# Kernel optimization log

Measured on AMD Instinct MI355X. Metric: run time of the kernel, lower is better.

The kernel has to match this reference:

```python
import jax, jax.numpy as jnp
import numpy as np

N, D, H, N_HEADS = 2048, 512, 512, 16

def setup_inputs() -> dict:
    key = jax.random.key(0)
    k1, k2, k3 = jax.random.split(key, 3)
    inputs = jax.random.normal(k1, (N, D), dtype=jnp.float32)
    idx = jax.random.randint(k2, (N,), 0, N_HEADS, dtype=jnp.int64)
    weights = jax.random.normal(k3, (N_HEADS, D, H), dtype=jnp.float32)
    biases = jnp.zeros((N_HEADS, H), dtype=jnp.float32)
    return {"inputs": inputs, "idx": idx, "weights": weights, "biases": biases}

def reference(inputs, idx, weights, biases):
    # per-sample weight gather: (N, D, H) then batched vec-mat: (N, 1, D) @ (N, D, H) -> (N, H)
    w = weights[idx]            # (N, D, H)  -- the redundant materialized gather
    b = biases[idx]             # (N, H)
    return jnp.einsum('nd,ndh->nh', inputs, w) + b
```

## Files before the change

kernel.cpp:

```cpp
#include <hip/hip_runtime.h>


#define N_SAMPLES 2048
#define DIM       512
#define HDIM      512
#define N_HEADS   16
#define SH        32
#define BPITCH    520

typedef __attribute__((ext_vector_type(8))) short bf16x8;
typedef __attribute__((ext_vector_type(4))) float floatx4;

__device__ inline unsigned short f2bf_rne(float f) {
    union { float f; unsigned u; } v; v.f = f;
    return (unsigned short)((v.u + 0x7FFFu + ((v.u >> 16) & 1u)) >> 16);
}
__device__ inline unsigned bfpack_rne(float lo, float hi) {
    return (unsigned)f2bf_rne(lo) | ((unsigned)f2bf_rne(hi) << 16);
}

__global__ __launch_bounds__(256) void xconv(const float* __restrict__ x,
                                             unsigned* __restrict__ xb) {
    const int i = blockIdx.x * 256 + threadIdx.x;
    const float4 v0 = *(const float4*)(x + i * 8);
    const float4 v1 = *(const float4*)(x + i * 8 + 4);
    uint4 o;
    o.x = bfpack_rne(v0.x, v0.y);
    o.y = bfpack_rne(v0.z, v0.w);
    o.z = bfpack_rne(v1.x, v1.y);
    o.w = bfpack_rne(v1.z, v1.w);
    *(uint4*)(xb + i * 4) = o;
}

__global__ __launch_bounds__(256, 2) void fused(
    const unsigned short* __restrict__ xb,
    const int*   __restrict__ idx,
    const float* __restrict__ w,
    const float* __restrict__ bias,
    float*       __restrict__ out)
{
    __shared__ unsigned short Bl[SH * BPITCH];
    __shared__ unsigned short slist[N_SAMPLES];
    __shared__ int wcnt[4];

    const int bid  = blockIdx.x;
    const int head = bid >> 4;
    const int h0   = (bid & 15) * SH;
    const int t    = threadIdx.x;
    const int wave = t >> 6;
    const int lane = t & 63;
    const int l16  = lane & 15;
    const int quad = lane >> 4;

    int myidx[8];
    #pragma unroll
    for (int c = 0; c < 8; ++c)
        myidx[c] = idx[(wave * 8 + c) * 64 + lane];

    const int hh = (t & 7) * 4;
    const int dg = t >> 3;
    const float* wg = w + (size_t)head * DIM * HDIM + h0;
    float4 q[16];
    #pragma unroll
    for (int s = 0; s < 16; ++s)
        q[s] = *(const float4*)(wg + (size_t)(dg * 16 + s) * HDIM + hh);

    unsigned long long masks[8];
    {
        int mycnt = 0;
        #pragma unroll
        for (int c = 0; c < 8; ++c) {
            masks[c] = __ballot(myidx[c] == head);
            mycnt += __popcll(masks[c]);
        }
        if (lane == 0) wcnt[wave] = mycnt;
    }
    __syncthreads();
    int cnt = 0, base = 0;
    #pragma unroll
    for (int i = 0; i < 4; ++i) { if (i < wave) base += wcnt[i]; cnt += wcnt[i]; }
    {
        int pos = base;
        #pragma unroll
        for (int c = 0; c < 8; ++c) {
            const unsigned long long m = masks[c];
            if (m & (1ull << lane)) {
                const int rank = __popcll(m & ((1ull << lane) - 1ull));
                slist[pos + rank] = (unsigned short)((wave * 8 + c) * 64 + lane);
            }
            pos += __popcll(m);
        }
    }

    #pragma unroll
    for (int p = 0; p < 8; ++p) {
        const int d = dg * 16 + 2 * p;
        const float4 qa = q[2 * p], qb = q[2 * p + 1];
        *(unsigned*)&Bl[(hh + 0) * BPITCH + d] = bfpack_rne(qa.x, qb.x);
        *(unsigned*)&Bl[(hh + 1) * BPITCH + d] = bfpack_rne(qa.y, qb.y);
        *(unsigned*)&Bl[(hh + 2) * BPITCH + d] = bfpack_rne(qa.z, qb.z);
        *(unsigned*)&Bl[(hh + 3) * BPITCH + d] = bfpack_rne(qa.w, qb.w);
    }
    __syncthreads();

    const int   mt  = (cnt + 15) >> 4;
    const float bv0 = bias[head * HDIM + h0 + l16];
    const float bv1 = bias[head * HDIM + h0 + 16 + l16];

    int j = wave;
    bf16x8 a[16];
    if (j < mt) {
        const int mg  = j * 16 + l16;
        const int row = slist[mg < cnt ? mg : cnt - 1];
        const unsigned short* ap = xb + (size_t)row * DIM + quad * 8;
        #pragma unroll
        for (int ks = 0; ks < 16; ++ks) a[ks] = *(const bf16x8*)(ap + ks * 32);
    }
    for (; j < mt; j += 4) {
        bf16x8 an[16];
        const int jn = j + 4;
        if (jn < mt) {
            const int mg  = jn * 16 + l16;
            const int row = slist[mg < cnt ? mg : cnt - 1];
            const unsigned short* ap = xb + (size_t)row * DIM + quad * 8;
            #pragma unroll
            for (int ks = 0; ks < 16; ++ks) an[ks] = *(const bf16x8*)(ap + ks * 32);
        }

        floatx4 acc0 = {0.f, 0.f, 0.f, 0.f};
        floatx4 acc1 = {0.f, 0.f, 0.f, 0.f};
        #pragma unroll
        for (int ks = 0; ks < 16; ++ks) {
            const bf16x8 b0 = *(const bf16x8*)&Bl[l16 * BPITCH + ks * 32 + quad * 8];
            const bf16x8 b1 = *(const bf16x8*)&Bl[(16 + l16) * BPITCH + ks * 32 + quad * 8];
            acc0 = __builtin_amdgcn_mfma_f32_16x16x32_bf16(a[ks], b0, acc0, 0, 0, 0);
            acc1 = __builtin_amdgcn_mfma_f32_16x16x32_bf16(a[ks], b1, acc1, 0, 0, 0);
        }

        #pragma unroll
        for (int r = 0; r < 4; ++r) {
            const int mm = j * 16 + quad * 4 + r;
            if (mm < cnt) {
                const int rg = slist[mm];
                out[(size_t)rg * HDIM + h0 + l16]      = acc0[r] + bv0;
                out[(size_t)rg * HDIM + h0 + 16 + l16] = acc1[r] + bv1;
            }
        }

        #pragma unroll
        for (int ks = 0; ks < 16; ++ks) a[ks] = an[ks];
    }
}

extern "C" void kernel_launch(void* const* d_in, const int* in_sizes, int n_in,
                              void* d_out, int out_size, void* d_ws, size_t ws_size,
                              hipStream_t stream) {
    const float* x   = (const float*)d_in[0];
    const int*   idx = (const int*)  d_in[1];
    const float* w   = (const float*)d_in[2];
    const float* b   = (const float*)d_in[3];
    float*       out = (float*)d_out;

    unsigned* xb = (unsigned*)d_ws;

    xconv<<<512, 256, 0, stream>>>(x, xb);
    fused<<<N_HEADS * (HDIM / SH), 256, 0, stream>>>((const unsigned short*)xb, idx, w, b, out);
}
```

Measured before the change: 86.77 us.

## Fuse fp32-to-bf16 input conversion into GEMM kernel and use 512-thread blocks

Removes the separate xconv pre-pass and instead loads fp32 input rows directly in the main kernel, converting them to bf16 right before the MFMA. Blocks grow from 4 to 8 waves, so the per-thread weight staging and index scanning work is halved. The software prefetch of the next A tile is dropped. The aim is to save one kernel launch and the round trip through the workspace, at the cost of reading twice as many bytes of x per block and exposing load latency inside the MFMA loop.

After: 85.52 us. Within noise of the previous version (-1.4%).

```diff
diff --git a/kernel.cpp b/kernel.cpp
--- a/kernel.cpp
+++ b/kernel.cpp
@@ -19,21 +19,8 @@
     return (unsigned)f2bf_rne(lo) | ((unsigned)f2bf_rne(hi) << 16);
 }
 
-__global__ __launch_bounds__(256) void xconv(const float* __restrict__ x,
-                                             unsigned* __restrict__ xb) {
-    const int i = blockIdx.x * 256 + threadIdx.x;
-    const float4 v0 = *(const float4*)(x + i * 8);
-    const float4 v1 = *(const float4*)(x + i * 8 + 4);
-    uint4 o;
-    o.x = bfpack_rne(v0.x, v0.y);
-    o.y = bfpack_rne(v0.z, v0.w);
-    o.z = bfpack_rne(v1.x, v1.y);
-    o.w = bfpack_rne(v1.z, v1.w);
-    *(uint4*)(xb + i * 4) = o;
-}
-
-__global__ __launch_bounds__(256, 2) void fused(
-    const unsigned short* __restrict__ xb,
+__global__ __launch_bounds__(512, 2) void fused(
+    const float* __restrict__ x,
     const int*   __restrict__ idx,
     const float* __restrict__ w,
     const float* __restrict__ bias,
@@ -41,7 +28,7 @@
 {
     __shared__ unsigned short Bl[SH * BPITCH];
     __shared__ unsigned short slist[N_SAMPLES];
-    __shared__ int wcnt[4];
+    __shared__ int wcnt[8];
 
     const int bid  = blockIdx.x;
     const int head = bid >> 4;
@@ -52,24 +39,24 @@
     const int l16  = lane & 15;
     const int quad = lane >> 4;
 
-    int myidx[8];
+    int myidx[4];
     #pragma unroll
-    for (int c = 0; c < 8; ++c)
-        myidx[c] = idx[(wave * 8 + c) * 64 + lane];
+    for (int c = 0; c < 4; ++c)
+        myidx[c] = idx[(wave * 4 + c) * 64 + lane];
 
     const int hh = (t & 7) * 4;
     const int dg = t >> 3;
     const float* wg = w + (size_t)head * DIM * HDIM + h0;
-    float4 q[16];
+    float4 q[8];
     #pragma unroll
-    for (int s = 0; s < 16; ++s)
-        q[s] = *(const float4*)(wg + (size_t)(dg * 16 + s) * HDIM + hh);
+    for (int s = 0; s < 8; ++s)
+        q[s] = *(const float4*)(wg + (size_t)(dg * 8 + s) * HDIM + hh);
 
-    unsigned long long masks[8];
+    unsigned long long masks[4];
     {
         int mycnt = 0;
         #pragma unroll
-        for (int c = 0; c < 8; ++c) {
+        for (int c = 0; c < 4; ++c) {
             masks[c] = __ballot(myidx[c] == head);
             mycnt += __popcll(masks[c]);
         }
@@ -78,23 +65,23 @@
     __syncthreads();
     int cnt = 0, base = 0;
     #pragma unroll
-    for (int i = 0; i < 4; ++i) { if (i < wave) base += wcnt[i]; cnt += wcnt[i]; }
+    for (int i = 0; i < 8; ++i) { if (i < wave) base += wcnt[i]; cnt += wcnt[i]; }
     {
         int pos = base;
         #pragma unroll
-        for (int c = 0; c < 8; ++c) {
+        for (int c = 0; c < 4; ++c) {
             const unsigned long long m = masks[c];
             if (m & (1ull << lane)) {
                 const int rank = __popcll(m & ((1ull << lane) - 1ull));
-                slist[pos + rank] = (unsigned short)((wave * 8 + c) * 64 + lane);
+                slist[pos + rank] = (unsigned short)((wave * 4 + c) * 64 + lane);
             }
             pos += __popcll(m);
         }
     }
 
     #pragma unroll
-    for (int p = 0; p < 8; ++p) {
-        const int d = dg * 16 + 2 * p;
+    for (int p = 0; p < 4; ++p) {
+        const int d = dg * 8 + 2 * p;
         const float4 qa = q[2 * p], qb = q[2 * p + 1];
         *(unsigned*)&Bl[(hh + 0) * BPITCH + d] = bfpack_rne(qa.x, qb.x);
         *(unsigned*)&Bl[(hh + 1) * BPITCH + d] = bfpack_rne(qa.y, qb.y);
@@ -107,34 +94,26 @@
     const float bv0 = bias[head * HDIM + h0 + l16];
     const float bv1 = bias[head * HDIM + h0 + 16 + l16];
 
-    int j = wave;
-    bf16x8 a[16];
-    if (j < mt) {
+    for (int j = wave; j < mt; j += 8) {
         const int mg  = j * 16 + l16;
         const int row = slist[mg < cnt ? mg : cnt - 1];
-        const unsigned short* ap = xb + (size_t)row * DIM + quad * 8;
-        #pragma unroll
-        for (int ks = 0; ks < 16; ++ks) a[ks] = *(const bf16x8*)(ap + ks * 32);
-    }
-    for (; j < mt; j += 4) {
-        bf16x8 an[16];
-        const int jn = j + 4;
-        if (jn < mt) {
-            const int mg  = jn * 16 + l16;
-            const int row = slist[mg < cnt ? mg : cnt - 1];
-            const unsigned short* ap = xb + (size_t)row * DIM + quad * 8;
-            #pragma unroll
-            for (int ks = 0; ks < 16; ++ks) an[ks] = *(const bf16x8*)(ap + ks * 32);
-        }
+        const float* ap = x + (size_t)row * DIM + quad * 8;
 
         floatx4 acc0 = {0.f, 0.f, 0.f, 0.f};
         floatx4 acc1 = {0.f, 0.f, 0.f, 0.f};
         #pragma unroll
         for (int ks = 0; ks < 16; ++ks) {
+            const float4 v0 = *(const float4*)(ap + ks * 32);
+            const float4 v1 = *(const float4*)(ap + ks * 32 + 4);
+            union { bf16x8 v; unsigned u[4]; } A;
+            A.u[0] = bfpack_rne(v0.x, v0.y);
+            A.u[1] = bfpack_rne(v0.z, v0.w);
+            A.u[2] = bfpack_rne(v1.x, v1.y);
+            A.u[3] = bfpack_rne(v1.z, v1.w);
             const bf16x8 b0 = *(const bf16x8*)&Bl[l16 * BPITCH + ks * 32 + quad * 8];
             const bf16x8 b1 = *(const bf16x8*)&Bl[(16 + l16) * BPITCH + ks * 32 + quad * 8];
-            acc0 = __builtin_amdgcn_mfma_f32_16x16x32_bf16(a[ks], b0, acc0, 0, 0, 0);
-            acc1 = __builtin_amdgcn_mfma_f32_16x16x32_bf16(a[ks], b1, acc1, 0, 0, 0);
+            acc0 = __builtin_amdgcn_mfma_f32_16x16x32_bf16(A.v, b0, acc0, 0, 0, 0);
+            acc1 = __builtin_amdgcn_mfma_f32_16x16x32_bf16(A.v, b1, acc1, 0, 0, 0);
         }
 
         #pragma unroll
@@ -146,9 +125,6 @@
                 out[(size_t)rg * HDIM + h0 + 16 + l16] = acc1[r] + bv1;
             }
         }
-
-        #pragma unroll
-        for (int ks = 0; ks < 16; ++ks) a[ks] = an[ks];
     }
 }
 
@@ -160,9 +136,7 @@
     const float* w   = (const float*)d_in[2];
     const float* b   = (const float*)d_in[3];
     float*       out = (float*)d_out;
+    (void)d_ws; (void)ws_size;
 
-    unsigned* xb = (unsigned*)d_ws;
-
-    xconv<<<512, 256, 0, stream>>>(x, xb);
-    fused<<<N_HEADS * (HDIM / SH), 256, 0, stream>>>((const unsigned short*)xb, idx, w, b, out);
+    fused<<<N_HEADS * (HDIM / SH), 512, 0, stream>>>(x, idx, w, b, out);
 }
```
